# Kernel tuning notes

Measured on AMD Instinct MI355X. Metric: run time of the kernel, lower is better.

Reference implementation:

```python
import jax, jax.numpy as jnp
import numpy as np

MAX_REL = 64  # max_relative_position
LN_EPS = 1e-5


def _relative_positions(seq_len):
    r = jnp.arange(seq_len)
    rel = jnp.clip(r[None, :] - r[:, None], -MAX_REL, MAX_REL) + MAX_REL
    return rel  # [S, S] int32 in [0, 2*MAX_REL]


def setup_inputs() -> dict:
    key = jax.random.key(0)
    ks = jax.random.split(key, 8)
    B, S, H = 8, 1024, 128
    sd = 1.0 / np.sqrt(H)
    return {
        "x": jax.random.normal(ks[0], (B, S, H), jnp.float32),
        "Wq": jax.random.normal(ks[1], (H, H), jnp.float32) * sd,
        "bq": jnp.zeros((H,), jnp.float32),
        "Wk": jax.random.normal(ks[2], (H, H), jnp.float32) * sd,
        "bk": jnp.zeros((H,), jnp.float32),
        "Wv": jax.random.normal(ks[3], (H, H), jnp.float32) * sd,
        "bv": jnp.zeros((H,), jnp.float32),
        "rel_k": jax.random.normal(ks[4], (2 * MAX_REL + 1, H), jnp.float32),
        "rel_v": jax.random.normal(ks[5], (2 * MAX_REL + 1, H), jnp.float32),
        "Wo": jax.random.normal(ks[6], (H, H), jnp.float32) * sd,
        "bo": jnp.zeros((H,), jnp.float32),
        "gamma": jnp.ones((H,), jnp.float32),
        "beta": jnpp if False else jnp.zeros((H,), jnp.float32),
    }


def reference(x, Wq, bq, Wk, bk, Wv, bv, rel_k, rel_v, Wo, bo, gamma, beta):
    B, S, H = x.shape
    scale = jnp.sqrt(jnp.asarray(H, x.dtype))

    q = x @ Wq + bq  # [B,S,H]
    k = x @ Wk + bk
    v = x @ Wv + bv

    scores = jnp.einsum("bih,bjh->bij", q, k) / scale  # [B,S,S]

    relpos = _relative_positions(S)            # [S,S] int
    rk = rel_k[relpos]                          # [S,S,H] gather
    scores = scores + jnp.einsum("bih,ijh->bij", q, rk)

    attn = jax.nn.softmax(scores, axis=-1)      # dropout = identity (eval)

    ctx = jnp.einsum("bij,bjh->bih", attn, v)
    rv = rel_v[relpos]                          # [S,S,H] gather
    ctx = ctx + jnp.einsum("bij,ijh->bih", attn, rv)

    out = ctx @ Wo + bo

    # residual + LayerNorm
    y = out + x
    mu = jnp.mean(y, axis=-1, keepdims=True)
    var = jnp.mean(jnp.square(y - mu), axis=-1, keepdims=True)
    y = (y - mu) * jax.lax.rsqrt(var + LN_EPS) * gamma + beta
    return y, attn
```

## Files before the change

kernel.cpp:

```cpp
#include <hip/hip_runtime.h>

constexpr int Bn = 8, Sn = 1024, Hn = 128, Rn = 129, RLD = 132;
constexpr float INV_SCALE = 0.088388347648318447f;
constexpr size_t YEL = (size_t)Bn * Sn * Hn;

typedef short bf16x8 __attribute__((ext_vector_type(8)));
typedef short v4s __attribute__((ext_vector_type(4)));
typedef float f32x4 __attribute__((ext_vector_type(4)));
typedef int v4i __attribute__((ext_vector_type(4)));

__device__ __forceinline__ float bf2f(short s) {
    unsigned u = ((unsigned)(unsigned short)s) << 16;
    float f; __builtin_memcpy(&f, &u, 4); return f;
}
__device__ __forceinline__ short f2bf(float f) {
    unsigned u; __builtin_memcpy(&u, &f, 4);
    unsigned r = (u + 0x7fffu + ((u >> 16) & 1u)) >> 16;
    return (short)(r & 0xffffu);
}

__device__ __forceinline__ void gll16(const short* g, short* l) {
    __builtin_amdgcn_global_load_lds(
        (const __attribute__((address_space(1))) void*)g,
        (__attribute__((address_space(3))) void*)l, 16, 0, 0);
}

__global__ __launch_bounds__(384) void build_tables(
    const float* __restrict__ rel_k, const float* __restrict__ rel_v,
    const float* __restrict__ Wo,
    short* __restrict__ relcat, short* __restrict__ BcatT)
{
    if (blockIdx.x < Rn) {
        const int p = blockIdx.x, c = threadIdx.x;
        const int j = (c < 256) ? (c & 127) : (c - 256);
        float v = rel_k[p * Hn + j];
        short h = f2bf(v);
        relcat[p * 384 + c] = (c < 256) ? h : f2bf(v - bf2f(h));
    } else {
        int idx = (blockIdx.x - Rn) * 384 + threadIdx.x;
        if (idx < 320 * 128) {
            int k = idx >> 7, n = idx & 127;
            float v;
            if (k < 128) v = Wo[k * Hn + n];
            else if (k < 257) {
                int p = k - 128; float a = 0.f;
                for (int h = 0; h < Hn; ++h) a += rel_v[p * Hn + h] * Wo[h * Hn + n];
                v = a;
            } else v = 0.f;
            BcatT[n * 320 + k] = f2bf(v);
        }
    }
}

__global__ __launch_bounds__(256) void proj(
    const float* __restrict__ X,
    const float* __restrict__ Wq, const float* __restrict__ bq,
    const float* __restrict__ Wk, const float* __restrict__ bk,
    const float* __restrict__ Wv, const float* __restrict__ bv,
    short* __restrict__ qh, short* __restrict__ qcat,
    short* __restrict__ kh, short* __restrict__ vT)
{
    __shared__ float xs[64][128];
    __shared__ float wsm[32][128];
    const int tid = threadIdx.x;
    const int sel = blockIdx.y;
    const int row0 = blockIdx.x * 64;
    const float* W = (sel == 0) ? Wq : (sel == 1) ? Wk : Wv;
    const float* bias = (sel == 0) ? bq : (sel == 1) ? bk : bv;

#pragma unroll
    for (int it = 0; it < 8; ++it) {
        int u = tid + it * 256;
        int r = u >> 5, c4 = (u & 31) * 4;
        *(float4*)&xs[r][c4] = *(const float4*)(X + (size_t)(row0 + r) * 128 + c4);
    }

    const int rg = tid >> 5, cg = tid & 31;
    float acc[8][4] = {};
    for (int kc = 0; kc < 128; kc += 32) {
#pragma unroll
        for (int it = 0; it < 4; ++it) {
            int u = tid + it * 256;
            int kk = u >> 5, c4 = (u & 31) * 4;
            *(float4*)&wsm[kk][c4] = *(const float4*)(W + (size_t)(kc + kk) * 128 + c4);
        }
        __syncthreads();
#pragma unroll 8
        for (int kk = 0; kk < 32; ++kk) {
            float wv[4];
#pragma unroll
            for (int c = 0; c < 4; ++c) wv[c] = wsm[kk][cg + c * 32];
#pragma unroll
            for (int r = 0; r < 8; ++r) {
                float xv = xs[rg * 8 + r][kc + kk];
#pragma unroll
                for (int c = 0; c < 4; ++c) acc[r][c] += xv * wv[c];
            }
        }
        __syncthreads();
    }

#pragma unroll
    for (int c = 0; c < 4; ++c) {
        int col = cg + c * 32;
        float bv2 = bias[col];
#pragma unroll
        for (int r = 0; r < 8; ++r) {
            int row = row0 + rg * 8 + r;
            float v = acc[r][c] + bv2;
            short h = f2bf(v);
            if (sel == 0) {
                qh[(size_t)row * 128 + col] = h;
                qcat[(size_t)row * 256 + col] = h;
                qcat[(size_t)row * 256 + 128 + col] = f2bf(v - bf2f(h));
            } else if (sel == 1) {
                kh[(size_t)row * 128 + col] = h;
            } else {
                int b = row >> 10, i = row & (Sn - 1);
                vT[(size_t)b * 131072 + (size_t)col * 1024 + i] = h;
            }
        }
    }
}

__global__ __launch_bounds__(256) void qrel_gemm(
    const short* __restrict__ qcat, const short* __restrict__ relcat,
    float* __restrict__ qrel)
{
    __shared__ short As[64][72];
    __shared__ short Bs[64][72];
    const int tid = threadIdx.x;
    const int wave = tid >> 6, lane = tid & 63;
    const int quad = lane >> 4, l15 = lane & 15;
    const int row0 = blockIdx.x * 64, col0 = blockIdx.y * 64;

    f32x4 acc[4] = {};
    for (int kc = 0; kc < 384; kc += 64) {
#pragma unroll
        for (int it = 0; it < 2; ++it) {
            int u = tid + it * 256;
            int r = u >> 3, c8 = (u & 7) * 8;
            int srcc = kc + c8;
            if (srcc >= 256) srcc -= 256;
            *(v4i*)&As[r][c8] = *(const v4i*)(qcat + (size_t)(row0 + r) * 256 + srcc);
        }
#pragma unroll
        for (int it = 0; it < 2; ++it) {
            int u = tid + it * 256;
            int r = u >> 3, c8 = (u & 7) * 8;
            v4i val = {0, 0, 0, 0};
            if (col0 + r < Rn)
                val = *(const v4i*)(relcat + (size_t)(col0 + r) * 384 + kc + c8);
            *(v4i*)&Bs[r][c8] = val;
        }
        __syncthreads();
#pragma unroll
        for (int ks = 0; ks < 64; ks += 32) {
            bf16x8 af = *(const bf16x8*)&As[wave * 16 + l15][ks + quad * 8];
#pragma unroll
            for (int nt = 0; nt < 4; ++nt) {
                bf16x8 bf = *(const bf16x8*)&Bs[nt * 16 + l15][ks + quad * 8];
                acc[nt] = __builtin_amdgcn_mfma_f32_16x16x32_bf16(af, bf, acc[nt], 0, 0, 0);
            }
        }
        __syncthreads();
    }
    const int rloc0 = wave * 16 + quad * 4;
#pragma unroll
    for (int nt = 0; nt < 4; ++nt) {
        int col = col0 + nt * 16 + l15;
#pragma unroll
        for (int r = 0; r < 4; ++r) {
            if (col < Rn)
                qrel[(size_t)(row0 + rloc0 + r) * RLD + col] = acc[nt][r];
        }
    }
}

__global__ __launch_bounds__(512, 4) void fused_attn(
    const short* __restrict__ qh, const short* __restrict__ kh,
    const short* __restrict__ vT, const float* __restrict__ qrel_g,
    const short* __restrict__ BcatT,
    const float* __restrict__ X, const float* __restrict__ bo,
    const float* __restrict__ gamma, const float* __restrict__ beta,
    float* __restrict__ attn_g, float* __restrict__ y_g)
{
    __shared__ __align__(16) char smem[78848];
    short* bufS = (short*)smem;
    short* Pb   = (short*)(smem + 32768);
    short* CtxA = (short*)(smem + 65792);
    float* QrL  = (float*)(smem + 65792);
    float* redM = (float*)(smem + 76800);
    float* redS = redM + 128;
    float* redL = redS + 128;
    float* redH = redL + 128;

    const int tid = threadIdx.x;
    const int w = tid >> 6, lane = tid & 63;
    const int quad = lane >> 4, l15 = lane & 15;
    const int lb = blockIdx.x + (blockIdx.z << 6);
    const int bz = lb & 7;
    const int row0 = (lb >> 3) << 4;
    const size_t grow0 = (size_t)bz * Sn + row0;

    const short* khb  = kh + (size_t)bz * Sn * 128;
    const short* vtb0 = vT + (size_t)bz * 131072;

#pragma unroll
    for (int rr = 0; rr < 2; ++rr) {
        int r = w * 2 + rr;
        const float* src = qrel_g + (grow0 + r) * RLD;
        QrL[r * 132 + lane] = src[lane];
        QrL[r * 132 + 64 + lane] = src[64 + lane];
        if (lane < 4) QrL[r * 132 + 128 + lane] = src[128 + lane];
    }

    bf16x8 afr[4];
#pragma unroll
    for (int kk = 0; kk < 4; ++kk)
        afr[kk] = *(const bf16x8*)(qh + (grow0 + l15) * 128 + kk * 32 + quad * 8);

    auto stage_kh = [&](int kt2) {
        const short* base = khb + (size_t)((kt2 >> 1) * 128) * 128 + (kt2 & 1) * 64;
        short* dst = bufS + (kt2 & 1) * 8192;
#pragma unroll
        for (int it = 0; it < 2; ++it) {
            int g = tid + it * 512;
            int r = g >> 3, c = g & 7;
            gll16(base + r * 128 + ((c ^ (r & 7)) * 8), dst + g * 8);
        }
    };
    auto stage_v = [&](int kc2) {
        const short* base = vtb0 + (kc2 >> 1) * 128 + (kc2 & 1) * 64;
        short* dst = bufS + (kc2 & 1) * 8192;
#pragma unroll
        for (int it = 0; it < 2; ++it) {
            int g = tid + it * 512;
            int r = g >> 3, c = g & 7;
            gll16(base + r * 1024 + ((c ^ (r & 7)) * 8), dst + g * 8);
        }
    };

    stage_kh(0);
    __syncthreads();
    f32x4 acc[8] = {};
#pragma unroll
    for (int kt2 = 0; kt2 < 16; ++kt2) {
        if (kt2 < 15) stage_kh(kt2 + 1);
        const short* hb = bufS + (kt2 & 1) * 8192;
        const int rb = w * 16 + l15;
#pragma unroll
        for (int kk = 0; kk < 2; ++kk) {
            int j = (kk * 4 + quad) ^ (l15 & 7);
            bf16x8 b = *(const bf16x8*)(hb + rb * 64 + j * 8);
            acc[kt2 >> 1] = __builtin_amdgcn_mfma_f32_16x16x32_bf16(
                afr[(kt2 & 1) * 2 + kk], b, acc[kt2 >> 1], 0, 0, 0);
        }
        __syncthreads();
    }

    stage_v(0);

    float mx[4];
#pragma unroll
    for (int r = 0; r < 4; ++r) {
        int lr = quad * 4 + r, i = row0 + lr;
        float m = -3.4e38f;
#pragma unroll
        for (int kt = 0; kt < 8; ++kt) {
            int col = kt * 128 + w * 16 + l15;
            int d = col - i; d = (d < -64) ? -64 : (d > 64 ? 64 : d);
            float v = acc[kt][r] * INV_SCALE + QrL[lr * 132 + d + 64];
            acc[kt][r] = v;
            m = fmaxf(m, v);
        }
#pragma unroll
        for (int msk = 1; msk < 16; msk <<= 1) m = fmaxf(m, __shfl_xor(m, msk));
        if (l15 == 0) redM[lr * 8 + w] = m;
    }
    __syncthreads();
#pragma unroll
    for (int r = 0; r < 4; ++r) {
        int lr = quad * 4 + r;
        float m = redM[lr * 8];
#pragma unroll
        for (int j = 1; j < 8; ++j) m = fmaxf(m, redM[lr * 8 + j]);
        mx[r] = m;
    }

#pragma unroll
    for (int r = 0; r < 4; ++r) {
        int lr = quad * 4 + r, i = row0 + lr;
        float s = 0.f, lo = 0.f, hi = 0.f;
#pragma unroll
        for (int kt = 0; kt < 8; ++kt) {
            float e = __expf(acc[kt][r] - mx[r]);
            acc[kt][r] = e;
            s += e;
            int col = kt * 128 + w * 16 + l15;
            lo += (col <= i - 64) ? e : 0.f;
            hi += (col >= i + 64) ? e : 0.f;
        }
#pragma unroll
        for (int msk = 1; msk < 16; msk <<= 1) {
            s += __shfl_xor(s, msk);
            lo += __shfl_xor(lo, msk);
            hi += __shfl_xor(hi, msk);
        }
        if (l15 == 0) { redS[lr * 8 + w] = s; redL[lr * 8 + w] = lo; redH[lr * 8 + w] = hi; }
    }
    __syncthreads();

#pragma unroll
    for (int r = 0; r < 4; ++r) {
        int lr = quad * 4 + r;
        float s = 0.f;
#pragma unroll
        for (int j = 0; j < 8; ++j) s += redS[lr * 8 + j];
        float inv = 1.0f / s;
#pragma unroll
        for (int kt = 0; kt < 8; ++kt) {
            int col = kt * 128 + w * 16 + l15;
            Pb[lr * 1032 + col] = f2bf(acc[kt][r] * inv);
        }
    }
    __syncthreads();

    {
        float* ab = attn_g + grow0 * Sn;
#pragma unroll
        for (int it = 0; it < 8; ++it) {
            int u = tid + it * 512;
            int r = u >> 8, c4 = (u & 255) * 4;
            v4s pv = *(const v4s*)&Pb[r * 1032 + c4];
            f32x4 o;
            o[0] = bf2f(pv[0]); o[1] = bf2f(pv[1]);
            o[2] = bf2f(pv[2]); o[3] = bf2f(pv[3]);
            __builtin_nontemporal_store(o, (f32x4*)(ab + (size_t)r * Sn + c4));
        }
    }

    f32x4 cacc = {};
#pragma unroll
    for (int kc2 = 0; kc2 < 16; ++kc2) {
        if (kc2 < 15) stage_v(kc2 + 1);
        const short* hb = bufS + (kc2 & 1) * 8192;
        const int rb = w * 16 + l15;
#pragma unroll
        for (int kk = 0; kk < 2; ++kk) {
            bf16x8 a = *(const bf16x8*)&Pb[l15 * 1032 + kc2 * 64 + kk * 32 + quad * 8];
            int j = (kk * 4 + quad) ^ (l15 & 7);
            bf16x8 b = *(const bf16x8*)(hb + rb * 64 + j * 8);
            cacc = __builtin_amdgcn_mfma_f32_16x16x32_bf16(a, b, cacc, 0, 0, 0);
        }
        __syncthreads();
    }

#pragma unroll
    for (int r = 0; r < 4; ++r)
        CtxA[(quad * 4 + r) * 344 + w * 16 + l15] = f2bf(cacc[r]);
#pragma unroll
    for (int rr = 0; rr < 2; ++rr) {
        int lr = w * 2 + rr, i = row0 + lr;
        float s = 0.f, lo = 0.f, hi = 0.f;
#pragma unroll
        for (int j = 0; j < 8; ++j) {
            s += redS[lr * 8 + j]; lo += redL[lr * 8 + j]; hi += redH[lr * 8 + j];
        }
        float inv = 1.0f / s;
        float v0;
        if (lane == 0) v0 = lo * inv;
        else { int c = i + lane - 64; v0 = (c >= 0 && c < Sn) ? bf2f(Pb[lr * 1032 + c]) : 0.f; }
        CtxA[lr * 344 + 128 + lane] = f2bf(v0);
        int c1 = i + lane;
        CtxA[lr * 344 + 192 + lane] = (c1 < Sn) ? Pb[lr * 1032 + c1] : (short)0;
        CtxA[lr * 344 + 256 + lane] = (lane == 0) ? f2bf(hi * inv) : (short)0;
    }
    __syncthreads();

    f32x4 yacc = {};
    const short* bcb = BcatT + (size_t)(w * 16 + l15) * 320;
#pragma unroll
    for (int ch = 0; ch < 3; ++ch) {
        const int nkk = (ch == 2) ? 2 : 4;
#pragma unroll
        for (int kk = 0; kk < 4; ++kk) {
            if (kk >= nkk) break;
            bf16x8 a = *(const bf16x8*)&CtxA[l15 * 344 + ch * 128 + kk * 32 + quad * 8];
            bf16x8 b = *(const bf16x8*)(bcb + ch * 128 + kk * 32 + quad * 8);
            yacc = __builtin_amdgcn_mfma_f32_16x16x32_bf16(a, b, yacc, 0, 0, 0);
        }
    }

    const int col = w * 16 + l15;
    const float bov = bo[col], gv = gamma[col], bev = beta[col];
    float vv[4];
#pragma unroll
    for (int r = 0; r < 4; ++r) {
        int lr = quad * 4 + r;
        vv[r] = yacc[r] + bov + X[(grow0 + lr) * 128 + col];
    }
#pragma unroll
    for (int r = 0; r < 4; ++r) {
        float s = vv[r];
#pragma unroll
        for (int msk = 1; msk < 16; msk <<= 1) s += __shfl_xor(s, msk);
        if (l15 == 0) redM[(quad * 4 + r) * 8 + w] = s;
    }
    __syncthreads();
    float mu[4];
#pragma unroll
    for (int r = 0; r < 4; ++r) {
        int lr = quad * 4 + r;
        float s = 0.f;
#pragma unroll
        for (int j = 0; j < 8; ++j) s += redM[lr * 8 + j];
        mu[r] = s * (1.f / 128.f);
    }
#pragma unroll
    for (int r = 0; r < 4; ++r) {
        float d = vv[r] - mu[r];
        float s = d * d;
#pragma unroll
        for (int msk = 1; msk < 16; msk <<= 1) s += __shfl_xor(s, msk);
        if (l15 == 0) redS[(quad * 4 + r) * 8 + w] = s;
    }
    __syncthreads();
#pragma unroll
    for (int r = 0; r < 4; ++r) {
        int lr = quad * 4 + r;
        float s = 0.f;
#pragma unroll
        for (int j = 0; j < 8; ++j) s += redS[lr * 8 + j];
        float inv = rsqrtf(s * (1.f / 128.f) + 1e-5f);
        float yv = (vv[r] - mu[r]) * inv * gv + bev;
        __builtin_nontemporal_store(yv, &y_g[(grow0 + lr) * 128 + col]);
    }
}

extern "C" void kernel_launch(void* const* d_in, const int* in_sizes, int n_in,
                              void* d_out, int out_size, void* d_ws, size_t ws_size,
                              hipStream_t stream) {
    const float* x     = (const float*)d_in[0];
    const float* Wq    = (const float*)d_in[1];
    const float* bq    = (const float*)d_in[2];
    const float* Wk    = (const float*)d_in[3];
    const float* bk    = (const float*)d_in[4];
    const float* Wv    = (const float*)d_in[5];
    const float* bv    = (const float*)d_in[6];
    const float* rel_k = (const float*)d_in[7];
    const float* rel_v = (const float*)d_in[8];
    const float* Wo    = (const float*)d_in[9];
    const float* bo    = (const float*)d_in[10];
    const float* gamma = (const float*)d_in[11];
    const float* beta  = (const float*)d_in[12];

    char* ws = (char*)d_ws;
    short* qh     = (short*)(ws + 0);
    short* kh     = (short*)(ws + 2097152);
    short* vT     = (short*)(ws + 4194304);
    short* qcat   = (short*)(ws + 6291456);
    float* qrel   = (float*)(ws + 10485760);
    short* relcat = (short*)(ws + 14811136);
    short* BcatT  = (short*)(ws + 14910464);

    float* y_out = (float*)d_out;
    float* attn  = (float*)d_out + YEL;

    build_tables<<<dim3(Rn + 107), 384, 0, stream>>>(rel_k, rel_v, Wo, relcat, BcatT);
    proj<<<dim3(128, 3), 256, 0, stream>>>(x, Wq, bq, Wk, bk, Wv, bv, qh, qcat, kh, vT);
    qrel_gemm<<<dim3(128, 3), 256, 0, stream>>>(qcat, relcat, qrel);

    fused_attn<<<dim3(64, 1, Bn), 512, 0, stream>>>(
        qh, kh, vT, qrel, BcatT, x, bo, gamma, beta, attn, y_out);
}
```

Measured before the change: 157.8 us.

## Fuse q·rel_k GEMM into attention kernel and drop separate qh buffer

Removes the standalone qrel_gemm kernel and computes the per-row q·rel_k projection inside fused_attn with MFMA, writing results straight into shared memory. The q-high bf16 fragments are now read from qcat instead of a duplicate qh buffer, so proj no longer writes qh. This saves one kernel launch plus the global write and read of the qrel intermediate. In exchange, each attention block now does extra MFMA work and relcat reads before its main loop, and wave 0 carries an extra tile for the 129th column, which adds some imbalance.

Result: no change. 155.8 us (-1.3%).

```diff
diff --git a/kernel.cpp b/kernel.cpp
--- a/kernel.cpp
+++ b/kernel.cpp
@@ -1,6 +1,6 @@
 #include <hip/hip_runtime.h>
 
-constexpr int Bn = 8, Sn = 1024, Hn = 128, Rn = 129, RLD = 132;
+constexpr int Bn = 8, Sn = 1024, Hn = 128, Rn = 129;
 constexpr float INV_SCALE = 0.088388347648318447f;
 constexpr size_t YEL = (size_t)Bn * Sn * Hn;
 
@@ -57,8 +57,7 @@
     const float* __restrict__ Wq, const float* __restrict__ bq,
     const float* __restrict__ Wk, const float* __restrict__ bk,
     const float* __restrict__ Wv, const float* __restrict__ bv,
-    short* __restrict__ qh, short* __restrict__ qcat,
-    short* __restrict__ kh, short* __restrict__ vT)
+    short* __restrict__ qcat, short* __restrict__ kh, short* __restrict__ vT)
 {
     __shared__ float xs[64][128];
     __shared__ float wsm[32][128];
@@ -110,7 +109,6 @@
             float v = acc[r][c] + bv2;
             short h = f2bf(v);
             if (sel == 0) {
-                qh[(size_t)row * 128 + col] = h;
                 qcat[(size_t)row * 256 + col] = h;
                 qcat[(size_t)row * 256 + 128 + col] = f2bf(v - bf2f(h));
             } else if (sel == 1) {
@@ -123,63 +121,9 @@
     }
 }
 
-__global__ __launch_bounds__(256) void qrel_gemm(
-    const short* __restrict__ qcat, const short* __restrict__ relcat,
-    float* __restrict__ qrel)
-{
-    __shared__ short As[64][72];
-    __shared__ short Bs[64][72];
-    const int tid = threadIdx.x;
-    const int wave = tid >> 6, lane = tid & 63;
-    const int quad = lane >> 4, l15 = lane & 15;
-    const int row0 = blockIdx.x * 64, col0 = blockIdx.y * 64;
-
-    f32x4 acc[4] = {};
-    for (int kc = 0; kc < 384; kc += 64) {
-#pragma unroll
-        for (int it = 0; it < 2; ++it) {
-            int u = tid + it * 256;
-            int r = u >> 3, c8 = (u & 7) * 8;
-            int srcc = kc + c8;
-            if (srcc >= 256) srcc -= 256;
-            *(v4i*)&As[r][c8] = *(const v4i*)(qcat + (size_t)(row0 + r) * 256 + srcc);
-        }
-#pragma unroll
-        for (int it = 0; it < 2; ++it) {
-            int u = tid + it * 256;
-            int r = u >> 3, c8 = (u & 7) * 8;
-            v4i val = {0, 0, 0, 0};
-            if (col0 + r < Rn)
-                val = *(const v4i*)(relcat + (size_t)(col0 + r) * 384 + kc + c8);
-            *(v4i*)&Bs[r][c8] = val;
-        }
-        __syncthreads();
-#pragma unroll
-        for (int ks = 0; ks < 64; ks += 32) {
-            bf16x8 af = *(const bf16x8*)&As[wave * 16 + l15][ks + quad * 8];
-#pragma unroll
-            for (int nt = 0; nt < 4; ++nt) {
-                bf16x8 bf = *(const bf16x8*)&Bs[nt * 16 + l15][ks + quad * 8];
-                acc[nt] = __builtin_amdgcn_mfma_f32_16x16x32_bf16(af, bf, acc[nt], 0, 0, 0);
-            }
-        }
-        __syncthreads();
-    }
-    const int rloc0 = wave * 16 + quad * 4;
-#pragma unroll
-    for (int nt = 0; nt < 4; ++nt) {
-        int col = col0 + nt * 16 + l15;
-#pragma unroll
-        for (int r = 0; r < 4; ++r) {
-            if (col < Rn)
-                qrel[(size_t)(row0 + rloc0 + r) * RLD + col] = acc[nt][r];
-        }
-    }
-}
-
 __global__ __launch_bounds__(512, 4) void fused_attn(
-    const short* __restrict__ qh, const short* __restrict__ kh,
-    const short* __restrict__ vT, const float* __restrict__ qrel_g,
+    const short* __restrict__ qcat, const short* __restrict__ kh,
+    const short* __restrict__ vT, const short* __restrict__ relcat,
     const short* __restrict__ BcatT,
     const float* __restrict__ X, const float* __restrict__ bo,
     const float* __restrict__ gamma, const float* __restrict__ beta,
@@ -206,20 +150,6 @@
     const short* khb  = kh + (size_t)bz * Sn * 128;
     const short* vtb0 = vT + (size_t)bz * 131072;
 
-#pragma unroll
-    for (int rr = 0; rr < 2; ++rr) {
-        int r = w * 2 + rr;
-        const float* src = qrel_g + (grow0 + r) * RLD;
-        QrL[r * 132 + lane] = src[lane];
-        QrL[r * 132 + 64 + lane] = src[64 + lane];
-        if (lane < 4) QrL[r * 132 + 128 + lane] = src[128 + lane];
-    }
-
-    bf16x8 afr[4];
-#pragma unroll
-    for (int kk = 0; kk < 4; ++kk)
-        afr[kk] = *(const bf16x8*)(qh + (grow0 + l15) * 128 + kk * 32 + quad * 8);
-
     auto stage_kh = [&](int kt2) {
         const short* base = khb + (size_t)((kt2 >> 1) * 128) * 128 + (kt2 & 1) * 64;
         short* dst = bufS + (kt2 & 1) * 8192;
@@ -242,7 +172,41 @@
     };
 
     stage_kh(0);
-    __syncthreads();
+
+    bf16x8 afr[4];
+#pragma unroll
+    for (int kk = 0; kk < 4; ++kk)
+        afr[kk] = *(const bf16x8*)(qcat + (grow0 + l15) * 256 + kk * 32 + quad * 8);
+
+    {
+        const short* aq = qcat + (grow0 + l15) * 256;
+        const short* br = relcat + (size_t)(w * 16 + l15) * 384;
+        const short* br2 = relcat + (size_t)(128 + l15) * 384;
+        f32x4 qacc = {};
+        f32x4 qacc2 = {};
+#pragma unroll
+        for (int ks = 0; ks < 12; ++ks) {
+            int koff = ks * 32 + quad * 8;
+            int srcc = (koff >= 256) ? koff - 256 : koff;
+            bf16x8 qa = *(const bf16x8*)(aq + srcc);
+            bf16x8 qb = *(const bf16x8*)(br + ks * 32 + quad * 8);
+            qacc = __builtin_amdgcn_mfma_f32_16x16x32_bf16(qa, qb, qacc, 0, 0, 0);
+            if (w == 0) {
+                bf16x8 qb2 = *(const bf16x8*)(br2 + ks * 32 + quad * 8);
+                qacc2 = __builtin_amdgcn_mfma_f32_16x16x32_bf16(qa, qb2, qacc2, 0, 0, 0);
+            }
+        }
+#pragma unroll
+        for (int r = 0; r < 4; ++r)
+            QrL[(quad * 4 + r) * 132 + w * 16 + l15] = qacc[r];
+        if (w == 0 && l15 == 0) {
+#pragma unroll
+            for (int r = 0; r < 4; ++r)
+                QrL[(quad * 4 + r) * 132 + 128] = qacc2[r];
+        }
+    }
+    __syncthreads();
+
     f32x4 acc[8] = {};
 #pragma unroll
     for (int kt2 = 0; kt2 < 16; ++kt2) {
@@ -456,21 +420,18 @@
     const float* beta  = (const float*)d_in[12];
 
     char* ws = (char*)d_ws;
-    short* qh     = (short*)(ws + 0);
-    short* kh     = (short*)(ws + 2097152);
-    short* vT     = (short*)(ws + 4194304);
-    short* qcat   = (short*)(ws + 6291456);
-    float* qrel   = (float*)(ws + 10485760);
-    short* relcat = (short*)(ws + 14811136);
-    short* BcatT  = (short*)(ws + 14910464);
+    short* kh     = (short*)(ws + 0);
+    short* vT     = (short*)(ws + 2097152);
+    short* qcat   = (short*)(ws + 4194304);
+    short* relcat = (short*)(ws + 8388608);
+    short* BcatT  = (short*)(ws + 8519680);
 
     float* y_out = (float*)d_out;
     float* attn  = (float*)d_out + YEL;
 
     build_tables<<<dim3(Rn + 107), 384, 0, stream>>>(rel_k, rel_v, Wo, relcat, BcatT);
-    proj<<<dim3(128, 3), 256, 0, stream>>>(x, Wq, bq, Wk, bk, Wv, bv, qh, qcat, kh, vT);
-    qrel_gemm<<<dim3(128, 3), 256, 0, stream>>>(qcat, relcat, qrel);
+    proj<<<dim3(128, 3), 256, 0, stream>>>(x, Wq, bq, Wk, bk, Wv, bv, qcat, kh, vT);
 
     fused_attn<<<dim3(64, 1, Bn), 512, 0, stream>>>(
-        qh, kh, vT, qrel, BcatT, x, bo, gamma, beta, attn, y_out);
-}
+        qcat, kh, vT, relcat, BcatT, x, bo, gamma, beta, attn, y_out);
+}
```
